# Kernel optimization log

Hardware: AMD Instinct MI355X
Metric: run time of the kernel (lower is better)

Reference implementation:

```python
import jax, jax.numpy as jnp
import numpy as np

B, C, N, D, H, HID, E, L = 4, 8, 1024, 256, 8, 768, 8192, 256
EPS = 1e-5


def rms(x, w):
    return x * jax.lax.rsqrt(jnp.mean(x * x, axis=-1, keepdims=True) + EPS) * w


def swiglu(x, w1, w2, w3):
    return (jax.nn.silu(x @ w1.T) * (x @ w3.T)) @ w2.T


def mha(x, in_w, in_b, out_w, out_b):
    # x: [BC, N, D]; torch MultiheadAttention with packed in_proj
    qkv = x @ in_w.T + in_b
    q, k, v = jnp.split(qkv, 3, axis=-1)
    dh = D // H
    sp = lambda t: t.reshape(t.shape[0], -1, H, dh).transpose(0, 2, 1, 3)
    q, k, v = sp(q), sp(k), sp(v)
    scores = jnp.einsum('bhqd,bhkd->bhqk', q, k) / np.sqrt(dh).astype(np.float32)
    a = jax.nn.softmax(scores, axis=-1)
    o = jnp.einsum('bhqk,bhkd->bhqd', a, v).transpose(0, 2, 1, 3).reshape(x.shape)
    return o @ out_w.T + out_b


def setup_inputs() -> dict:
    key = jax.random.key(0)
    ks = jax.random.split(key, 24)
    s = 0.02
    p = {}
    p['v'] = jax.random.normal(ks[0], (B, C, N, D), jnp.float32)
    src = jax.random.randint(ks[1], (E,), 0, N)
    dst = jax.random.randint(ks[2], (E,), 0, L)
    p['data_to_logical'] = jnp.stack([src, dst]).astype(jnp.int64)
    # transformer layer params
    p['attn_norm_w'] = jnp.ones((D,), jnp.float32)
    p['in_proj_w'] = jax.random.normal(ks[3], (3 * D, D), jnp.float32) * s
    p['in_proj_b'] = jnp.zeros((3 * D,), jnp.float32)
    p['out_w'] = jax.random.normal(ks[4], (D, D), jnp.float32) * s
    p['out_b'] = jnp.zeros((D,), jnp.float32)
    p['ffn_norm_w'] = jnp.ones((D,), jnp.float32)
    p['ffn_w1'] = jax.random.normal(ks[5], (HID, D), jnp.float32) * s
    p['ffn_w2'] = jax.random.normal(ks[6], (D, HID), jnp.float32) * s
    p['ffn_w3'] = jax.random.normal(ks[7], (HID, D), jnp.float32) * s
    # data_update = RMSNorm + SwiGLU
    p['du_norm_w'] = jnp.ones((D,), jnp.float32)
    p['du_w1'] = jax.random.normal(ks[8], (HID, D), jnp.float32) * s
    p['du_w2'] = jax.random.normal(ks[9], (D, HID), jnp.float32) * s
    p['du_w3'] = jax.random.normal(ks[10], (HID, D), jnp.float32) * s
    # logical_update = RMSNorm + SwiGLU
    p['lu_norm_w'] = jnp.ones((D,), jnp.float32)
    p['lu_w1'] = jax.random.normal(ks[11], (HID, D), jnp.float32) * s
    p['lu_w2'] = jax.random.normal(ks[12], (D, HID), jnp.float32) * s
    p['lu_w3'] = jax.random.normal(ks[13], (HID, D), jnp.float32) * s
    p['head_w'] = jax.random.normal(ks[14], (1, D), jnp.float32) * s
    p['head_b'] = jnp.zeros((1,), jnp.float32)
    return p


def reference(v, data_to_logical, attn_norm_w, in_proj_w, in_proj_b, out_w, out_b,
              ffn_norm_w, ffn_w1, ffn_w2, ffn_w3,
              du_norm_w, du_w1, du_w2, du_w3,
              lu_norm_w, lu_w1, lu_w2, lu_w3,
              head_w, head_b):
    x = v.reshape(B * C, N, D)
    # single FullyConnectedTransformerLayer (num_layers=1)
    a = mha(rms(x, attn_norm_w), in_proj_w, in_proj_b, out_w, out_b) + x
    x = swiglu(rms(a, ffn_norm_w), ffn_w1, ffn_w2, ffn_w3) + a
    x = x.reshape(B, C, N, D)
    # data update + tanh scatter activation
    x = jnp.tanh(swiglu(rms(x, du_norm_w), du_w1, du_w2, du_w3) + x)
    # gather along node dim, scatter-multiply into L logical nodes
    src, dst = data_to_logical[0], data_to_logical[1]
    gathered = x[:, :, src, :]                              # [B, C, E, D]
    l = jnp.ones((B, C, L, D), x.dtype).at[:, :, dst, :].multiply(gathered)
    l = swiglu(rms(l, lu_norm_w), lu_w1, lu_w2, lu_w3) + l
    return (l @ head_w.T + head_b).squeeze(-1)              # [B, C, L]
```

## Files before the change

kernel.cpp:

```cpp
#include <hip/hip_runtime.h>
#include <hip/hip_bf16.h>

#define Nn 1024
#define Dd 256
#define Ee 8192
#define Ll 256
#define BC 32
#define TOK 32768
#define LTOK 8192
#define EPSf 1e-5f
#define SCL2 0.2550348871963368f

typedef __hip_bfloat16 bf16;
typedef __attribute__((ext_vector_type(8))) short bf16x8;
typedef __attribute__((ext_vector_type(4))) short short4v;
typedef __attribute__((ext_vector_type(4))) float f32x4;
typedef __attribute__((ext_vector_type(16))) float f32x16;

__device__ __forceinline__ short f2bf(float v) {
    __hip_bfloat16 h = __float2bfloat16(v);
    return __builtin_bit_cast(short, h);
}
__device__ __forceinline__ float bf2f(short b) {
    unsigned u = ((unsigned)(unsigned short)b) << 16;
    return __builtin_bit_cast(float, u);
}

__device__ __forceinline__ void gload_lds16(const short* g, short* l) {
    __builtin_amdgcn_global_load_lds(
        (const __attribute__((address_space(1))) void*)g,
        (__attribute__((address_space(3))) void*)l, 16, 0, 0);
}

#define SB_INW  0
#define SB_OUTW 196608
#define SB_F1   262144
#define SB_F3   458752
#define SB_F2   655360
#define SB_D1   851968
#define SB_D3   1048576
#define SB_D2   1245184
#define SB_L1   1441792
#define SB_L3   1638400
#define SB_L2   1835008

#define F_ANORM 0
#define F_INB   256
#define F_OUTB  1024
#define F_FNORM 1280
#define F_DNORM 1536
#define F_LNORM 1792
#define F_HW    2048
#define F_HB    2304

__global__ __launch_bounds__(256) void detect_kernel(const unsigned* __restrict__ anw,
                                                     const int* __restrict__ d2l,
                                                     int* __restrict__ flags) {
    __shared__ int nz;
    int t = threadIdx.x;
    if (t == 0) nz = 0;
    __syncthreads();
    int any = 0;
    for (int i = t * 2 + 1; i < 16384; i += 512)
        if (d2l[i] != 0) any = 1;
    if (any) atomicOr(&nz, 1);
    __syncthreads();
    if (t == 0) {
        flags[0] = (anw[0] == 0x3F800000u) ? 1 : 0;
        flags[1] = nz;
    }
}

struct WcastArgs { const void* src[11]; int off[11]; int n[11]; };
__global__ __launch_bounds__(256) void wcast_kernel(WcastArgs a, short* __restrict__ WB,
                                                    const int* __restrict__ flags) {
    int j = blockIdx.y;
    int i = blockIdx.x * 256 + threadIdx.x;
    if (i >= a.n[j]) return;
    short* d = WB + a.off[j];
    float v = flags[0] ? ((const float*)a.src[j])[i]
                       : bf2f(((const short*)a.src[j])[i]);
    if (j == 0 && (i >> 8) < 256) v *= SCL2;
    d[i] = f2bf(v);
}

struct PcastArgs { const void* src[8]; int off[8]; int n[8]; };
__global__ __launch_bounds__(256) void pcast_kernel(PcastArgs a, float* __restrict__ WF,
                                                    const int* __restrict__ flags) {
    int j = blockIdx.y;
    int i = blockIdx.x * 256 + threadIdx.x;
    if (i >= a.n[j]) return;
    float* d = WF + a.off[j];
    float v = flags[0] ? ((const float*)a.src[j])[i]
                       : bf2f(((const short*)a.src[j])[i]);
    if (j == 1 && i < 256) v *= SCL2;
    d[i] = v;
}

__global__ __launch_bounds__(256) void normcast_in(const void* __restrict__ src,
                                                   size_t base,
                                                   const int* __restrict__ flags,
                                                   const float* __restrict__ nw,
                                                   float* __restrict__ X,
                                                   short* __restrict__ Xn) {
    int r = blockIdx.x, t = threadIdx.x;
    __shared__ float red[256];
    size_t il = (size_t)r * Dd + t;
    float x = flags[0] ? ((const float*)src)[base + il]
                       : bf2f(((const short*)src)[base + il]);
    X[il] = x;
    red[t] = x * x;
    __syncthreads();
    for (int o = 128; o > 0; o >>= 1) {
        if (t < o) red[t] += red[t + o];
        __syncthreads();
    }
    float rs = 1.0f / sqrtf(red[0] * (1.0f / Dd) + EPSf);
    Xn[il] = f2bf(x * rs * nw[t]);
}

__global__ __launch_bounds__(256) void normcast_kernel(const float* __restrict__ X,
                                                       const float* __restrict__ nw,
                                                       short* __restrict__ Xn) {
    int r = blockIdx.x, t = threadIdx.x;
    __shared__ float red[256];
    float x = X[(size_t)r * Dd + t];
    red[t] = x * x;
    __syncthreads();
    for (int o = 128; o > 0; o >>= 1) {
        if (t < o) red[t] += red[t + o];
        __syncthreads();
    }
    float rs = 1.0f / sqrtf(red[0] * (1.0f / Dd) + EPSf);
    Xn[(size_t)r * Dd + t] = f2bf(x * rs * nw[t]);
}

template <int NI>
__global__ __launch_bounds__(256) void mfma_gemm(
        const short* __restrict__ A,
        const short* __restrict__ Bw,
        void* Cp, int mode,
        const float* __restrict__ bias, const float* R,
        short* __restrict__ Vout,
        int M, int N, int K) {
    __shared__ short As[128][64];
    __shared__ short Bs[NI * 32][64];
    int tid = threadIdx.x;
    int rowbase = blockIdx.y * 128;
    int colbase = blockIdx.x * (NI * 32);
    int w = tid >> 6, l = tid & 63;
    int wm = (w & 1) * 64, wn = (w >> 1) * (NI * 16);
    int lm = l & 15, quad = l >> 4;

    f32x4 acc[4][NI];
    #pragma unroll
    for (int mi = 0; mi < 4; mi++)
        #pragma unroll
        for (int ni = 0; ni < NI; ni++)
            acc[mi][ni] = (f32x4){0.f, 0.f, 0.f, 0.f};

    int jr = tid >> 3, jc = tid & 7;
    int sc8 = (jc ^ (jr & 7)) * 8;
    int jc8 = jc * 8;
    int rsw = lm & 7;
    for (int k0 = 0; k0 < K; k0 += 64) {
        #pragma unroll
        for (int i = 0; i < 4; i++)
            gload_lds16(A + (size_t)(rowbase + jr + 32 * i) * K + k0 + sc8,
                        &As[jr + 32 * i][jc8]);
        #pragma unroll
        for (int i = 0; i < NI; i++)
            gload_lds16(Bw + (size_t)(colbase + jr + 32 * i) * K + k0 + sc8,
                        &Bs[jr + 32 * i][jc8]);
        __syncthreads();
        #pragma unroll
        for (int kk = 0; kk < 2; kk++) {
            int csw = ((kk * 4 + quad) ^ rsw) * 8;
            bf16x8 a[4], b[NI];
            #pragma unroll
            for (int mi = 0; mi < 4; mi++)
                a[mi] = *(const bf16x8*)&As[wm + mi * 16 + lm][csw];
            #pragma unroll
            for (int ni = 0; ni < NI; ni++)
                b[ni] = *(const bf16x8*)&Bs[wn + ni * 16 + lm][csw];
            #pragma unroll
            for (int mi = 0; mi < 4; mi++)
                #pragma unroll
                for (int ni = 0; ni < NI; ni++)
                    acc[mi][ni] = __builtin_amdgcn_mfma_f32_16x16x32_bf16(
                        a[mi], b[ni], acc[mi][ni], 0, 0, 0);
        }
        __syncthreads();
    }
    #pragma unroll
    for (int mi = 0; mi < 4; mi++) {
        #pragma unroll
        for (int ni = 0; ni < NI; ni++) {
            int gcol = colbase + wn + ni * 16 + lm;
            float bv = bias ? bias[gcol] : 0.0f;
            if (mode == 4 && gcol >= 512) {
                int hh = (gcol - 512) >> 5, dd = (gcol - 512) & 31;
                int grow0 = rowbase + wm + mi * 16 + quad * 4;
                int bz = grow0 >> 10, n0 = grow0 & 1023;
                short4v pk;
                #pragma unroll
                for (int r = 0; r < 4; r++)
                    pk[r] = f2bf(acc[mi][ni][r] + bv);
                *(short4v*)(Vout + (((size_t)((bz * 8 + hh) * 32 + dd)) << 10) + n0) = pk;
            } else {
                #pragma unroll
                for (int r = 0; r < 4; r++) {
                    int grow = rowbase + wm + mi * 16 + quad * 4 + r;
                    float v = acc[mi][ni][r] + bv;
                    if (mode == 4) {
                        ((short*)Cp)[(size_t)grow * 512 + gcol] = f2bf(v);
                    } else {
                        size_t o = (size_t)grow * N + gcol;
                        if (mode == 1) v += R[o];
                        else if (mode == 2) v = tanhf(v + R[o]);
                        if (mode == 3) ((short*)Cp)[o] = f2bf(v);
                        else           ((float*)Cp)[o] = v;
                    }
                }
            }
        }
    }
}

__global__ __launch_bounds__(256) void mfma_dual(
        const short* __restrict__ A,
        const short* __restrict__ Bw1, const short* __restrict__ Bw3,
        short* __restrict__ Hout, int M, int K) {
    __shared__ short As[128][64];
    __shared__ short Bs1[64][64];
    __shared__ short Bs3[64][64];
    int tid = threadIdx.x;
    int rowbase = blockIdx.y * 128;
    int colbase = blockIdx.x * 64;
    int w = tid >> 6, l = tid & 63;
    int wm = (w & 1) * 64, wn = (w >> 1) * 32;
    int lm = l & 15, quad = l >> 4;

    f32x4 acc1[4][2], acc3[4][2];
    #pragma unroll
    for (int mi = 0; mi < 4; mi++)
        #pragma unroll
        for (int ni = 0; ni < 2; ni++) {
            acc1[mi][ni] = (f32x4){0.f, 0.f, 0.f, 0.f};
            acc3[mi][ni] = (f32x4){0.f, 0.f, 0.f, 0.f};
        }

    int jr = tid >> 3, jc = tid & 7;
    int sc8 = (jc ^ (jr & 7)) * 8;
    int jc8 = jc * 8;
    int rsw = lm & 7;
    for (int k0 = 0; k0 < K; k0 += 64) {
        #pragma unroll
        for (int i = 0; i < 4; i++)
            gload_lds16(A + (size_t)(rowbase + jr + 32 * i) * K + k0 + sc8,
                        &As[jr + 32 * i][jc8]);
        #pragma unroll
        for (int i = 0; i < 2; i++) {
            gload_lds16(Bw1 + (size_t)(colbase + jr + 32 * i) * K + k0 + sc8,
                        &Bs1[jr + 32 * i][jc8]);
            gload_lds16(Bw3 + (size_t)(colbase + jr + 32 * i) * K + k0 + sc8,
                        &Bs3[jr + 32 * i][jc8]);
        }
        __syncthreads();
        #pragma unroll
        for (int kk = 0; kk < 2; kk++) {
            int csw = ((kk * 4 + quad) ^ rsw) * 8;
            bf16x8 a[4], b1[2], b3[2];
            #pragma unroll
            for (int mi = 0; mi < 4; mi++)
                a[mi] = *(const bf16x8*)&As[wm + mi * 16 + lm][csw];
            #pragma unroll
            for (int ni = 0; ni < 2; ni++) {
                b1[ni] = *(const bf16x8*)&Bs1[wn + ni * 16 + lm][csw];
                b3[ni] = *(const bf16x8*)&Bs3[wn + ni * 16 + lm][csw];
            }
            #pragma unroll
            for (int mi = 0; mi < 4; mi++)
                #pragma unroll
                for (int ni = 0; ni < 2; ni++) {
                    acc1[mi][ni] = __builtin_amdgcn_mfma_f32_16x16x32_bf16(
                        a[mi], b1[ni], acc1[mi][ni], 0, 0, 0);
                    acc3[mi][ni] = __builtin_amdgcn_mfma_f32_16x16x32_bf16(
                        a[mi], b3[ni], acc3[mi][ni], 0, 0, 0);
                }
        }
        __syncthreads();
    }
    #pragma unroll
    for (int mi = 0; mi < 4; mi++) {
        #pragma unroll
        for (int ni = 0; ni < 2; ni++) {
            int gcol = colbase + wn + ni * 16 + lm;
            #pragma unroll
            for (int r = 0; r < 4; r++) {
                int grow = rowbase + wm + mi * 16 + quad * 4 + r;
                float e = acc1[mi][ni][r];
                float h = (e / (1.0f + __expf(-e))) * acc3[mi][ni][r];
                Hout[(size_t)grow * 768 + gcol] = f2bf(h);
            }
        }
    }
}

__global__ __launch_bounds__(256) void mfma_out(
        const short* __restrict__ A, const short* __restrict__ Bw,
        int omode, const float* __restrict__ bias, const float* __restrict__ R,
        float* __restrict__ Xout, const float* __restrict__ nw,
        short* __restrict__ Xn, const float* __restrict__ hw,
        const float* __restrict__ hb, float* __restrict__ out,
        int M, int K) {
    __shared__ short As[64][64];
    __shared__ short Bs[256][64];
    __shared__ float red[64][2];
    int tid = threadIdx.x;
    int rowbase = blockIdx.x * 64;
    int w = tid >> 6, l = tid & 63;
    int wm = (w >> 1) * 32, wn = (w & 1) * 128;
    int lm = l & 15, quad = l >> 4;

    f32x4 acc[2][8];
    #pragma unroll
    for (int mi = 0; mi < 2; mi++)
        #pragma unroll
        for (int ni = 0; ni < 8; ni++)
            acc[mi][ni] = (f32x4){0.f, 0.f, 0.f, 0.f};

    int jr = tid >> 3, jc = tid & 7;
    int sc8 = (jc ^ (jr & 7)) * 8;
    int jc8 = jc * 8;
    int rsw = lm & 7;
    for (int k0 = 0; k0 < K; k0 += 64) {
        #pragma unroll
        for (int i = 0; i < 2; i++)
            gload_lds16(A + (size_t)(rowbase + jr + 32 * i) * K + k0 + sc8,
                        &As[jr + 32 * i][jc8]);
        #pragma unroll
        for (int i = 0; i < 8; i++)
            gload_lds16(Bw + (size_t)(jr + 32 * i) * K + k0 + sc8,
                        &Bs[jr + 32 * i][jc8]);
        __syncthreads();
        #pragma unroll
        for (int kk = 0; kk < 2; kk++) {
            int csw = ((kk * 4 + quad) ^ rsw) * 8;
            bf16x8 a[2], b[8];
            #pragma unroll
            for (int mi = 0; mi < 2; mi++)
                a[mi] = *(const bf16x8*)&As[wm + mi * 16 + lm][csw];
            #pragma unroll
            for (int ni = 0; ni < 8; ni++)
                b[ni] = *(const bf16x8*)&Bs[wn + ni * 16 + lm][csw];
            #pragma unroll
            for (int mi = 0; mi < 2; mi++)
                #pragma unroll
                for (int ni = 0; ni < 8; ni++)
                    acc[mi][ni] = __builtin_amdgcn_mfma_f32_16x16x32_bf16(
                        a[mi], b[ni], acc[mi][ni], 0, 0, 0);
        }
        __syncthreads();
    }

    float s[2][4] = {{0.f,0.f,0.f,0.f},{0.f,0.f,0.f,0.f}};
    #pragma unroll
    for (int mi = 0; mi < 2; mi++) {
        #pragma unroll
        for (int ni = 0; ni < 8; ni++) {
            int gcol = wn + ni * 16 + lm;
            float bb = bias ? bias[gcol] : 0.0f;
            float hv = (omode == 2) ? hw[gcol] : 0.0f;
            #pragma unroll
            for (int r = 0; r < 4; r++) {
                int grow = rowbase + wm + mi * 16 + quad * 4 + r;
                size_t o = (size_t)grow * 256 + gcol;
                float v = acc[mi][ni][r] + bb + R[o];
                if (omode == 1) v = tanhf(v);
                acc[mi][ni][r] = v;
                if (omode != 2) Xout[o] = v;
                if (omode == 0)      s[mi][r] += v * v;
                else if (omode == 2) s[mi][r] += v * hv;
            }
        }
    }

    if (omode == 0 || omode == 2) {
        #pragma unroll
        for (int mi = 0; mi < 2; mi++)
            #pragma unroll
            for (int r = 0; r < 4; r++) {
                float sv = s[mi][r];
                sv += __shfl_xor(sv, 1);
                sv += __shfl_xor(sv, 2);
                sv += __shfl_xor(sv, 4);
                sv += __shfl_xor(sv, 8);
                s[mi][r] = sv;
            }
        if (lm == 0) {
            #pragma unroll
            for (int mi = 0; mi < 2; mi++)
                #pragma unroll
                for (int r = 0; r < 4; r++)
                    red[wm + mi * 16 + quad * 4 + r][w & 1] = s[mi][r];
        }
        __syncthreads();
        if (omode == 0) {
            #pragma unroll
            for (int mi = 0; mi < 2; mi++) {
                float rs[4];
                #pragma unroll
                for (int r = 0; r < 4; r++) {
                    int wrow = wm + mi * 16 + quad * 4 + r;
                    rs[r] = 1.0f / sqrtf((red[wrow][0] + red[wrow][1]) *
                                         (1.0f / Dd) + EPSf);
                }
                #pragma unroll
                for (int ni = 0; ni < 8; ni++) {
                    int gcol = wn + ni * 16 + lm;
                    float nv = nw[gcol];
                    #pragma unroll
                    for (int r = 0; r < 4; r++) {
                        int grow = rowbase + wm + mi * 16 + quad * 4 + r;
                        Xn[(size_t)grow * 256 + gcol] =
                            f2bf(acc[mi][ni][r] * rs[r] * nv);
                    }
                }
            }
        } else {
            if ((w & 1) == 0 && lm == 0) {
                #pragma unroll
                for (int mi = 0; mi < 2; mi++)
                    #pragma unroll
                    for (int r = 0; r < 4; r++) {
                        int wrow = wm + mi * 16 + quad * 4 + r;
                        out[rowbase + wrow] = red[wrow][0] + red[wrow][1] + hb[0];
                    }
            }
        }
    }
}

__global__ __launch_bounds__(256) void attn_mfma(const short* __restrict__ QKb,
                                                 const short* __restrict__ VtG,
                                                 short* __restrict__ Acb, int nbz) {
    int pair = blockIdx.x;
    int h = pair / nbz, bz = pair % nbz;
    int qt = blockIdx.y;
    int tid = threadIdx.x;
    int w = tid >> 6, l = tid & 63;
    int l31 = l & 31, hi = l >> 5;

    __shared__ short Ks[128][40];
    __shared__ short Vt[32][136];

    const short* base = QKb + (size_t)bz * Nn * 512;
    const short* vbase = VtG + (((size_t)(bz * 8 + h)) << 15);
    int q0 = qt * 128 + w * 32;

    bf16x8 qfrag[2];
    #pragma unroll
    for (int s = 0; s < 2; s++)
        qfrag[s] = *(const bf16x8*)(base +
            (size_t)(q0 + l31) * 512 + h * 32 + s * 16 + hi * 8);

    short onesv = 0x3F80;
    bf16x8 onesfrag = {onesv, onesv, onesv, onesv, onesv, onesv, onesv, onesv};

    f32x16 Oacc, Lacc;
    #pragma unroll
    for (int r = 0; r < 16; r++) { Oacc[r] = 0.f; Lacc[r] = 0.f; }

    for (int kt = 0; kt < 8; kt++) {
        int k0 = kt * 128;
        #pragma unroll
        for (int i = 0; i < 2; i++) {
            int idx = tid + 256 * i;
            int r = idx >> 2, c8 = (idx & 3) * 8;
            *(uint4*)&Ks[r][c8] =
                *(const uint4*)(base + (size_t)(k0 + r) * 512 + 256 + h * 32 + c8);
        }
        #pragma unroll
        for (int i = 0; i < 2; i++) {
            int idx = tid + 256 * i;
            int d = idx >> 4, c8 = (idx & 15) * 8;
            *(uint4*)&Vt[d][c8] =
                *(const uint4*)(vbase + ((size_t)d << 10) + k0 + c8);
        }
        __syncthreads();

        #pragma unroll
        for (int sub = 0; sub < 4; sub++) {
            f32x16 sacc;
            #pragma unroll
            for (int r = 0; r < 16; r++) sacc[r] = 0.f;
            #pragma unroll
            for (int s = 0; s < 2; s++) {
                bf16x8 kfrag = *(const bf16x8*)&Ks[sub * 32 + l31][s * 16 + hi * 8];
                sacc = __builtin_amdgcn_mfma_f32_32x32x16_bf16(
                    kfrag, qfrag[s], sacc, 0, 0, 0);
            }
            #pragma unroll
            for (int r = 0; r < 16; r++)
                sacc[r] = __builtin_amdgcn_exp2f(sacc[r]);
            #pragma unroll
            for (int s = 0; s < 2; s++) {
                unsigned pa, pb, pc, pd;
                asm("v_cvt_pk_bf16_f32 %0, %1, %2" : "=v"(pa)
                    : "v"(sacc[8 * s + 0]), "v"(sacc[8 * s + 1]));
                asm("v_cvt_pk_bf16_f32 %0, %1, %2" : "=v"(pc)
                    : "v"(sacc[8 * s + 2]), "v"(sacc[8 * s + 3]));
                asm("v_cvt_pk_bf16_f32 %0, %1, %2" : "=v"(pb)
                    : "v"(sacc[8 * s + 4]), "v"(sacc[8 * s + 5]));
                asm("v_cvt_pk_bf16_f32 %0, %1, %2" : "=v"(pd)
                    : "v"(sacc[8 * s + 6]), "v"(sacc[8 * s + 7]));
                asm("v_permlane32_swap_b32 %0, %1" : "+v"(pa), "+v"(pb));
                asm("v_permlane32_swap_b32 %0, %1" : "+v"(pc), "+v"(pd));
                uint4 pu = {pa, pc, pb, pd};
                bf16x8 pfrag = __builtin_bit_cast(bf16x8, pu);
                bf16x8 vfrag = *(const bf16x8*)&Vt[l31][sub * 32 + s * 16 + hi * 8];
                Oacc = __builtin_amdgcn_mfma_f32_32x32x16_bf16(
                    pfrag, vfrag, Oacc, 0, 0, 0);
                Lacc = __builtin_amdgcn_mfma_f32_32x32x16_bf16(
                    pfrag, onesfrag, Lacc, 0, 0, 0);
            }
        }
        __syncthreads();
    }

    #pragma unroll
    for (int r = 0; r < 16; r++) {
        int qrow = (r & 3) + 8 * (r >> 2) + 4 * hi;
        float v = Oacc[r] * __builtin_amdgcn_rcpf(Lacc[r]);
        Acb[((size_t)bz * Nn + q0 + qrow) * 256 + h * 32 + l31] = f2bf(v);
    }
}

__global__ __launch_bounds__(256) void bucket_kernel(const int* __restrict__ d2l,
                                                     const int* __restrict__ flags,
                                                     int* __restrict__ bkt_src,
                                                     int* __restrict__ bkt_off) {
    __shared__ int cnt[256];
    __shared__ int off[257];
    int t = threadIdx.x;
    cnt[t] = 0;
    __syncthreads();
    bool i32 = (flags[1] != 0);
    for (int e = t; e < Ee; e += 256) {
        int dst = i32 ? d2l[Ee + e] : d2l[2 * (Ee + e)];
        atomicAdd(&cnt[dst], 1);
    }
    __syncthreads();
    if (t == 0) {
        int s = 0;
        for (int i = 0; i < 256; i++) { off[i] = s; s += cnt[i]; }
        off[256] = s;
    }
    __syncthreads();
    bkt_off[t] = off[t];
    if (t == 0) bkt_off[256] = off[256];
    cnt[t] = off[t];
    __syncthreads();
    for (int e = t; e < Ee; e += 256) {
        int dst = i32 ? d2l[Ee + e] : d2l[2 * (Ee + e)];
        int src = i32 ? d2l[e] : d2l[2 * e];
        int pos = atomicAdd(&cnt[dst], 1);
        bkt_src[pos] = src;
    }
}

__global__ __launch_bounds__(256) void scatter_kernel(const float* __restrict__ X,
                                                      const int* __restrict__ bkt_src,
                                                      const int* __restrict__ bkt_off,
                                                      float* __restrict__ Lb,
                                                      int donorm,
                                                      const float* __restrict__ nw,
                                                      short* __restrict__ Xn) {
    __shared__ float red[256];
    int bc = blockIdx.x;
    int row = blockIdx.y;
    int t = threadIdx.x;
    int s0 = bkt_off[row], s1 = bkt_off[row + 1];
    const float* Xb = X + (size_t)bc * Nn * Dd;
    float acc = 1.0f;
    for (int i = s0; i < s1; i++) {
        int src = bkt_src[i];
        acc *= Xb[(size_t)src * Dd + t];
    }
    size_t o = ((size_t)bc * Ll + row) * Dd + t;
    Lb[o] = acc;
    if (donorm) {
        red[t] = acc * acc;
        __syncthreads();
        for (int of = 128; of > 0; of >>= 1) {
            if (t < of) red[t] += red[t + of];
            __syncthreads();
        }
        float rs = 1.0f / sqrtf(red[0] * (1.0f / Dd) + EPSf);
        Xn[o] = f2bf(acc * rs * nw[t]);
    }
}

extern "C" void kernel_launch(void* const* d_in, const int* in_sizes, int n_in,
                              void* d_out, int out_size, void* d_ws, size_t ws_size,
                              hipStream_t stream) {
    const int* d2l = (const int*)d_in[1];
    float* out = (float*)d_out;

    float* ws = (float*)d_ws;
    size_t o_wb  = 0;
    size_t o_wf  = o_wb + 1048576;
    size_t o_x   = o_wf + 4096;
    size_t o_lb  = o_x + 8388608;
    size_t o_bkt = o_lb + 2097152;
    size_t o_bof = o_bkt + 8192;
    size_t o_flg = o_bof + 257;
    size_t o_sc  = o_flg + 3;

    int CH = 4096;
    for (int cand = 32768; cand > 4096; cand >>= 1) {
        size_t need = (o_sc + (size_t)cand * 640) * 4;
        if (need + (1 << 20) <= ws_size) { CH = cand; break; }
    }
    int CHL = (CH < LTOK) ? CH : LTOK;

    short* WB  = (short*)(ws + o_wb);
    float* WF  = ws + o_wf;
    float* X   = ws + o_x;
    float* Lb  = ws + o_lb;
    int* bkt_src = (int*)(ws + o_bkt);
    int* bkt_off = (int*)(ws + o_bof);
    int* flags   = (int*)(ws + o_flg);
    float* SC  = ws + o_sc;

    short* Xnc  = (short*)SC;
    short* QKVb = (short*)SC + (size_t)CH * 256;
    short* VtG  = (short*)SC + (size_t)CH * 768;
    short* Acb  = (short*)SC + (size_t)CH * 1024;
    short* Hb   = (short*)SC + (size_t)CH * 256;

    const bool full  = (CH == TOK);
    const int  fullL = (CHL == LTOK);

    detect_kernel<<<1, 256, 0, stream>>>((const unsigned*)d_in[2], d2l, flags);

    WcastArgs wa = {
        {d_in[3], d_in[5], d_in[8], d_in[9], d_in[10], d_in[12],
         d_in[13], d_in[14], d_in[16], d_in[17], d_in[18]},
        {SB_INW, SB_OUTW, SB_F1, SB_F2, SB_F3, SB_D1, SB_D2, SB_D3,
         SB_L1, SB_L2, SB_L3},
        {196608, 65536, 196608, 196608, 196608, 196608, 196608, 196608,
         196608, 196608, 196608}};
    wcast_kernel<<<dim3(768, 11), 256, 0, stream>>>(wa, WB, flags);
    PcastArgs pa = {
        {d_in[2], d_in[4], d_in[6], d_in[7], d_in[11], d_in[15], d_in[19], d_in[20]},
        {F_ANORM, F_INB, F_OUTB, F_FNORM, F_DNORM, F_LNORM, F_HW, F_HB},
        {256, 768, 256, 256, 256, 256, 256, 1}};
    pcast_kernel<<<dim3(3, 8), 256, 0, stream>>>(pa, WF, flags);

    bucket_kernel<<<1, 256, 0, stream>>>(d2l, flags, bkt_src, bkt_off);

    const dim3 gIn(768 / 128, CH / 128);
    const dim3 gDual(768 / 64, CH / 128);
    const dim3 gDualL(768 / 64, CHL / 128);
    const int nbz = CH / Nn;

    for (int c = 0; c < TOK / CH; c++) {
        float* Xc = X + (size_t)c * CH * Dd;
        normcast_in<<<CH, 256, 0, stream>>>(d_in[0], (size_t)c * CH * Dd, flags,
                                            WF + F_ANORM, Xc, Xnc);
        mfma_gemm<4><<<gIn, 256, 0, stream>>>(Xnc, WB + SB_INW, QKVb, 4,
                                              WF + F_INB, nullptr, VtG,
                                              CH, 768, 256);
        attn_mfma<<<dim3(8 * nbz, 8), 256, 0, stream>>>(QKVb, VtG, Acb, nbz);
        mfma_out<<<CH / 64, 256, 0, stream>>>(Acb, WB + SB_OUTW, full ? 0 : 3,
                                              WF + F_OUTB, Xc, Xc,
                                              WF + F_FNORM, Xnc,
                                              nullptr, nullptr, nullptr,
                                              CH, 256);
    }

    for (int c = 0; c < TOK / CH; c++) {
        float* Xc = X + (size_t)c * CH * Dd;
        if (!full)
            normcast_kernel<<<CH, 256, 0, stream>>>(Xc, WF + F_FNORM, Xnc);
        mfma_dual<<<gDual, 256, 0, stream>>>(Xnc, WB + SB_F1, WB + SB_F3, Hb, CH, 256);
        mfma_out<<<CH / 64, 256, 0, stream>>>(Hb, WB + SB_F2, full ? 0 : 3,
                                              nullptr, Xc, Xc,
                                              WF + F_DNORM, Xnc,
                                              nullptr, nullptr, nullptr,
                                              CH, 768);
    }

    for (int c = 0; c < TOK / CH; c++) {
        float* Xc = X + (size_t)c * CH * Dd;
        if (!full)
            normcast_kernel<<<CH, 256, 0, stream>>>(Xc, WF + F_DNORM, Xnc);
        mfma_dual<<<gDual, 256, 0, stream>>>(Xnc, WB + SB_D1, WB + SB_D3, Hb, CH, 256);
        mfma_out<<<CH / 64, 256, 0, stream>>>(Hb, WB + SB_D2, 1,
                                              nullptr, Xc, Xc,
                                              nullptr, nullptr,
                                              nullptr, nullptr, nullptr,
                                              CH, 768);
    }

    scatter_kernel<<<dim3(BC, Ll), 256, 0, stream>>>(X, bkt_src, bkt_off, Lb,
                                                     fullL, WF + F_LNORM, Xnc);

    for (int c = 0; c < LTOK / CHL; c++) {
        float* Lc = Lb + (size_t)c * CHL * Dd;
        if (!fullL)
            normcast_kernel<<<CHL, 256, 0, stream>>>(Lc, WF + F_LNORM, Xnc);
        mfma_dual<<<gDualL, 256, 0, stream>>>(Xnc, WB + SB_L1, WB + SB_L3, Hb, CHL, 256);
        mfma_out<<<CHL / 64, 256, 0, stream>>>(Hb, WB + SB_L2, 2,
                                               nullptr, Lc, nullptr,
                                               nullptr, nullptr,
                                               WF + F_HW, WF + F_HB,
                                               out + (size_t)c * CHL,
                                               CHL, 768);
    }
}
```

Measured before the change: 578.9 us.

## Remap GEMM blocks across XCDs and double attention query tile per block

```diff
diff --git a/kernel.cpp b/kernel.cpp
--- a/kernel.cpp
+++ b/kernel.cpp
@@ -30,6 +30,16 @@
     __builtin_amdgcn_global_load_lds(
         (const __attribute__((address_space(1))) void*)g,
         (__attribute__((address_space(3))) void*)l, 16, 0, 0);
+}
+
+__device__ __forceinline__ void xcd_remap(int& bx, int& by) {
+    int gx = gridDim.x, nwg = gx * gridDim.y;
+    int lin = blockIdx.x + blockIdx.y * gx;
+    if ((nwg & 7) == 0) {
+        int cpx = nwg >> 3;
+        int nl = (lin & 7) * cpx + (lin >> 3);
+        bx = nl % gx; by = nl / gx;
+    } else { bx = blockIdx.x; by = blockIdx.y; }
 }
 
 #define SB_INW  0
@@ -146,8 +156,10 @@
     __shared__ short As[128][64];
     __shared__ short Bs[NI * 32][64];
     int tid = threadIdx.x;
-    int rowbase = blockIdx.y * 128;
-    int colbase = blockIdx.x * (NI * 32);
+    int bx, by;
+    xcd_remap(bx, by);
+    int rowbase = by * 128;
+    int colbase = bx * (NI * 32);
     int w = tid >> 6, l = tid & 63;
     int wm = (w & 1) * 64, wn = (w >> 1) * (NI * 16);
     int lm = l & 15, quad = l >> 4;
@@ -235,8 +247,10 @@
     __shared__ short Bs1[64][64];
     __shared__ short Bs3[64][64];
     int tid = threadIdx.x;
-    int rowbase = blockIdx.y * 128;
-    int colbase = blockIdx.x * 64;
+    int bx, by;
+    xcd_remap(bx, by);
+    int rowbase = by * 128;
+    int colbase = bx * 64;
     int w = tid >> 6, l = tid & 63;
     int wm = (w & 1) * 64, wn = (w >> 1) * 32;
     int lm = l & 15, quad = l >> 4;
@@ -442,7 +456,7 @@
     }
 }
 
-__global__ __launch_bounds__(256) void attn_mfma(const short* __restrict__ QKb,
+__global__ __launch_bounds__(512) void attn_mfma(const short* __restrict__ QKb,
                                                  const short* __restrict__ VtG,
                                                  short* __restrict__ Acb, int nbz) {
     int pair = blockIdx.x;
@@ -457,7 +471,7 @@
 
     const short* base = QKb + (size_t)bz * Nn * 512;
     const short* vbase = VtG + (((size_t)(bz * 8 + h)) << 15);
-    int q0 = qt * 128 + w * 32;
+    int q0 = qt * 256 + w * 32;
 
     bf16x8 qfrag[2];
     #pragma unroll
@@ -474,17 +488,13 @@
 
     for (int kt = 0; kt < 8; kt++) {
         int k0 = kt * 128;
-        #pragma unroll
-        for (int i = 0; i < 2; i++) {
-            int idx = tid + 256 * i;
-            int r = idx >> 2, c8 = (idx & 3) * 8;
+        {
+            int r = tid >> 2, c8 = (tid & 3) * 8;
             *(uint4*)&Ks[r][c8] =
                 *(const uint4*)(base + (size_t)(k0 + r) * 512 + 256 + h * 32 + c8);
         }
-        #pragma unroll
-        for (int i = 0; i < 2; i++) {
-            int idx = tid + 256 * i;
-            int d = idx >> 4, c8 = (idx & 15) * 8;
+        {
+            int d = tid >> 4, c8 = (tid & 15) * 8;
             *(uint4*)&Vt[d][c8] =
                 *(const uint4*)(vbase + ((size_t)d << 10) + k0 + c8);
         }
@@ -673,7 +683,7 @@
         mfma_gemm<4><<<gIn, 256, 0, stream>>>(Xnc, WB + SB_INW, QKVb, 4,
                                               WF + F_INB, nullptr, VtG,
                                               CH, 768, 256);
-        attn_mfma<<<dim3(8 * nbz, 8), 256, 0, stream>>>(QKVb, VtG, Acb, nbz);
+        attn_mfma<<<dim3(8 * nbz, 4), 512, 0, stream>>>(QKVb, VtG, Acb, nbz);
         mfma_out<<<CH / 64, 256, 0, stream>>>(Acb, WB + SB_OUTW, full ? 0 : 3,
                                               WF + F_OUTB, Xc, Xc,
                                               WF + F_FNORM, Xnc,
```

After: 535.7 us. -7.5%, faster.
